# Kernel optimization log

Hardware: AMD Instinct MI355X
Metric: run time of the kernel (lower is better)

## Reference

```python
import jax, jax.numpy as jnp
import numpy as np

N = 10000          # total nodes
N_AGENTS = 5000    # drones (x[:, -1] < 0)
E = 160000         # random edges (self-loops added in reference)
C_IN, H, C_HID, C_OUT = 16, 8, 128, 8
NEG_SLOPE = 0.2    # GATv2Conv default leaky_relu slope


def setup_inputs() -> dict:
    key = jax.random.key(0)
    ks = jax.random.split(key, 12)
    x = jax.random.normal(ks[0], (N, C_IN), dtype=jnp.float32)
    # last feature column encodes node type: <0 -> drone, >=0 -> goal
    type_col = jnp.where(jnp.arange(N) < N_AGENTS, -1.0, 1.0).astype(jnp.float32)
    x = x.at[:, -1].set(type_col)
    edge_index = jax.random.randint(ks[1], (2, E), 0, N, dtype=jnp.int32)
    s = 0.1  # glorot-ish scale
    return {
        "x": x,
        "edge_index": edge_index,
        "Wl1": s * jax.random.normal(ks[2], (C_IN, H * C_HID), jnp.float32),
        "bl1": jnp.zeros((H * C_HID,), jnp.float32),
        "Wr1": s * jax.random.normal(ks[3], (C_IN, H * C_HID), jnp.float32),
        "br1": jnp.zeros((H * C_HID,), jnp.float32),
        "att1": s * jax.random.normal(ks[4], (H, C_HID), jnp.float32),
        "b1": jnp.zeros((C_HID,), jnp.float32),
        "Wl2": s * jax.random.normal(ks[5], (C_HID, H * C_HID), jnp.float32),
        "bl2": jnp.zeros((H * C_HID,), jnp.float32),
        "Wr2": s * jax.random.normal(ks[6], (C_HID, H * C_HID), jnp.float32),
        "br2": jnp.zeros((H * C_HID,), jnp.float32),
        "att2": s * jax.random.normal(ks[7], (H, C_HID), jnp.float32),
        "b2": jnp.zeros((C_HID,), jnp.float32),
        "Wlin": s * jax.random.normal(ks[8], (C_HID, C_OUT), jnp.float32),
        "blin": jnp.zeros((C_OUT,), jnp.float32),
    }


def gatv2_conv(x, src, dst, Wl, bl, Wr, br, att, bias):
    """PyG GATv2Conv, heads=H, concat=False (head-mean), add_self_loops handled by caller."""
    n = x.shape[0]
    xl = (x @ Wl + bl).reshape(n, H, -1)   # [N,H,C] source transform
    xr = (x @ Wr + br).reshape(n, H, -1)   # [N,H,C] target transform
    e = jax.nn.leaky_relu(xl[src] + xr[dst], NEG_SLOPE)          # [E,H,C]
    alpha = jnp.einsum("ehc,hc->eh", e, att)                      # [E,H]
    # per-destination softmax over incoming edges
    m = jax.ops.segment_max(alpha, dst, num_segments=n)
    a = jnp.exp(alpha - m[dst])
    denom = jax.ops.segment_sum(a, dst, num_segments=n)
    a = a / (denom[dst] + 1e-16)
    out = jax.ops.segment_sum(xl[src] * a[:, :, None], dst, num_segments=n)  # [N,H,C]
    return out.mean(axis=1) + bias  # concat=False -> mean over heads


def reference(x, edge_index, Wl1, bl1, Wr1, br1, att1, b1,
              Wl2, bl2, Wr2, br2, att2, b2, Wlin, blin):
    n = x.shape[0]
    loops = jnp.arange(n, dtype=edge_index.dtype)
    src = jnp.concatenate([edge_index[0], loops])
    dst = jnp.concatenate([edge_index[1], loops])
    drone_mask = x[:, -1] < 0
    y = x  # bounds is None -> no division
    h = jax.nn.relu(gatv2_conv(y, src, dst, Wl1, bl1, Wr1, br1, att1, b1))
    h = jax.nn.relu(gatv2_conv(h, src, dst, Wl2, bl2, Wr2, br2, att2, b2))
    out = h @ Wlin + blin  # [N, C_OUT]
    idx = jnp.nonzero(drone_mask, size=N_AGENTS)[0]
    return out[idx]  # [N_AGENTS, C_OUT]
```

## Files before the change

kernel.cpp:

```cpp
#include <hip/hip_runtime.h>
#include <hip/hip_fp16.h>
#include <math.h>

#define N_NODES 10000
#define N_EDGES 160000
#define NAG     5000
#define HC      1024
#define CH      128
#define NEG     0.2f
#define BCAP    64

#define NSCAT   625
#define NGEMM   1256

typedef _Float16 f16x8 __attribute__((ext_vector_type(8)));
typedef _Float16 f16x2 __attribute__((ext_vector_type(2)));
typedef float f32x4 __attribute__((ext_vector_type(4)));

__device__ __forceinline__ __half2 pk_max(__half2 a, __half2 b) {
    __half2 r;
    asm volatile("v_pk_max_f16 %0, %1, %2" : "=v"(r) : "v"(a), "v"(b));
    return r;
}

__device__ __forceinline__ void edge_accum(float4 raw, const __half2* xr2, const __half2* att2,
                                           float& lsum, float* acc, bool valid) {
    __half2* hp = (__half2*)&raw;
    const __half2 neg2 = __float2half2_rn(NEG);
    float p = 0.f;
    #pragma unroll
    for (int j = 0; j < 4; j++) {
        __half2 z = __hadd2(hp[j], xr2[j]);
        __half2 lz = pk_max(z, __hmul2(z, neg2));
#if __has_builtin(__builtin_amdgcn_fdot2)
        p = __builtin_amdgcn_fdot2(*(f16x2*)&lz, *(const f16x2*)&att2[j], p, false);
#else
        float2 lf = __half22float2(lz);
        float2 af = __half22float2(att2[j]);
        p = fmaf(lf.x, af.x, p);
        p = fmaf(lf.y, af.y, p);
#endif
    }
    p += __shfl_xor(p, 1, 64);
    p += __shfl_xor(p, 2, 64);
    p += __shfl_xor(p, 4, 64);
    p += __shfl_xor(p, 8, 64);
    float w = valid ? __expf(p) : 0.f;
    lsum += w;
    #pragma unroll
    for (int j = 0; j < 4; j++) {
        acc[2 * j]     = fmaf(__low2float(hp[j]),  w, acc[2 * j]);
        acc[2 * j + 1] = fmaf(__high2float(hp[j]), w, acc[2 * j + 1]);
    }
}

template <int K, int KA, typename AT>
__device__ void gemm_tile(char* smem, int vt,
                          const AT* __restrict__ A,
                          const _Float16* __restrict__ Whl, const float* __restrict__ bl,
                          const _Float16* __restrict__ Whr, const float* __restrict__ br,
                          _Float16* __restrict__ xl, _Float16* __restrict__ xr,
                          int limitL, int limitR) {
    _Float16* ash = (_Float16*)smem;
    float (*eps)[68] = (float(*)[68])smem;
    __shared__ float bsh[256];
    const int AS = K + 8;
    int by = vt & 7;
    int rowblk = (vt >> 3) * 64;
    bool right = by >= 4;
    if (rowblk >= (right ? limitR : limitL)) return;
    const _Float16* Wh = right ? Whr : Whl;
    const float* bs    = right ? br : bl;
    _Float16* outp     = right ? xr : xl;
    int colbase = (by & 3) * 256;
    int t = threadIdx.x;
    int w = t >> 6, l = t & 63;
    int m = l & 15, q = l >> 4;

    bsh[t] = bs[colbase + t];
    for (int idx = t; idx < 64 * (K / 8); idx += 256) {
        int r  = idx / (K / 8);
        int c8 = (idx % (K / 8)) * 8;
        int row = rowblk + r;
        f16x8 hv = (f16x8){0, 0, 0, 0, 0, 0, 0, 0};
        if (row < N_NODES && c8 < KA) {
            if constexpr (sizeof(AT) == 2) {
                hv = *(const f16x8*)((const _Float16*)A + (size_t)row * KA + c8);
            } else {
                float4 v0 = *(const float4*)((const float*)A + (size_t)row * KA + c8);
                float4 v1 = *(const float4*)((const float*)A + (size_t)row * KA + c8 + 4);
                hv[0] = (_Float16)v0.x; hv[1] = (_Float16)v0.y; hv[2] = (_Float16)v0.z; hv[3] = (_Float16)v0.w;
                hv[4] = (_Float16)v1.x; hv[5] = (_Float16)v1.y; hv[6] = (_Float16)v1.z; hv[7] = (_Float16)v1.w;
            }
        }
        *(f16x8*)&ash[r * AS + c8] = hv;
    }
    __syncthreads();

    f32x4 acc[16];
    #pragma unroll
    for (int i = 0; i < 16; i++) acc[i] = (f32x4){0.f, 0.f, 0.f, 0.f};

    #pragma unroll
    for (int kq = 0; kq < K / 32; kq++) {
        f16x8 af = *(const f16x8*)&ash[(w * 16 + m) * AS + kq * 32 + q * 8];
        const _Float16* base = Wh + (((size_t)(kq * 64 + (colbase >> 4))) << 9) + l * 8;
        #pragma unroll
        for (int tile = 0; tile < 16; tile++) {
            f16x8 bf = *(const f16x8*)(base + ((size_t)tile << 9));
            acc[tile] = __builtin_amdgcn_mfma_f32_16x16x32_f16(af, bf, acc[tile], 0, 0, 0);
        }
    }

    float bv[16];
    #pragma unroll
    for (int tile = 0; tile < 16; tile++) bv[tile] = bsh[tile * 16 + m];

    for (int cgk = 0; cgk < 4; cgk++) {
        __syncthreads();
        #pragma unroll
        for (int tt = 0; tt < 4; tt++) {
            int tile = cgk * 4 + tt;
            int cl = tt * 16 + m;
            #pragma unroll
            for (int reg = 0; reg < 4; reg++)
                eps[w * 16 + q * 4 + reg][cl] = acc[tile][reg] + bv[tile];
        }
        __syncthreads();
        int colg = colbase + cgk * 64;
        int cc = (t & 15) * 4;
        #pragma unroll
        for (int it = 0; it < 4; it++) {
            int r = it * 16 + (t >> 4);
            int row = rowblk + r;
            if (row < N_NODES) {
                float4 v = *(const float4*)&eps[r][cc];
                __half2 h01 = __floats2half2_rn(v.x, v.y);
                __half2 h23 = __floats2half2_rn(v.z, v.w);
                float2 st;
                st.x = *(float*)&h01;
                st.y = *(float*)&h23;
                *(float2*)(outp + (size_t)row * HC + colg + cc) = st;
            }
        }
    }
}

template <int LAYER>
__device__ void gat_phase(char* smem, int ndst,
                          const __half* __restrict__ xl, const _Float16* __restrict__ xr,
                          const float* __restrict__ att, const float* __restrict__ bias,
                          const int* __restrict__ cnt, const int* __restrict__ srcs,
                          _Float16* __restrict__ h_out,
                          const float* __restrict__ Wlin, const float* __restrict__ blin,
                          float* __restrict__ out) {
    float* part  = (float*)smem;
    float* lpart = (float*)(smem + 8192);
    float* hrow  = (float*)(smem + 8256);
    int t = threadIdx.x;
    int slot = t >> 7;
    int c0 = (t & 127) * 8;

    for (int dstn = blockIdx.x; dstn < ndst; dstn += gridDim.x) {
        __half2 xr2[4], att2[4];
        {
            f16x8 xv = *(const f16x8*)(xr + (size_t)dstn * HC + c0);
            __half2* xp = (__half2*)&xv;
            xr2[0] = xp[0]; xr2[1] = xp[1]; xr2[2] = xp[2]; xr2[3] = xp[3];
            float4 b0 = *(const float4*)(att + c0);
            float4 b1 = *(const float4*)(att + c0 + 4);
            att2[0] = __floats2half2_rn(b0.x, b0.y);
            att2[1] = __floats2half2_rn(b0.z, b0.w);
            att2[2] = __floats2half2_rn(b1.x, b1.y);
            att2[3] = __floats2half2_rn(b1.z, b1.w);
        }

        float acc[8];
        #pragma unroll
        for (int j = 0; j < 8; j++) acc[j] = 0.f;
        float lsum = 0.f;

        int e0 = dstn << 6;
        int e1 = e0 + cnt[dstn];
        int e = e0;
        for (; e + 16 <= e1; e += 16) {
            int s[8];
            #pragma unroll
            for (int i = 0; i < 8; i++) s[i] = srcs[e + slot + 2 * i];
            float4 raw[8];
            #pragma unroll
            for (int i = 0; i < 8; i++) raw[i] = *(const float4*)(xl + (size_t)s[i] * HC + c0);
            #pragma unroll
            for (int i = 0; i < 8; i++) edge_accum(raw[i], xr2, att2, lsum, acc, true);
        }
        for (; e + 4 <= e1; e += 4) {
            int s[2];
            #pragma unroll
            for (int i = 0; i < 2; i++) s[i] = srcs[e + slot + 2 * i];
            float4 raw[2];
            #pragma unroll
            for (int i = 0; i < 2; i++) raw[i] = *(const float4*)(xl + (size_t)s[i] * HC + c0);
            #pragma unroll
            for (int i = 0; i < 2; i++) edge_accum(raw[i], xr2, att2, lsum, acc, true);
        }
        for (; e < e1; e += 2) {
            int ee = e + slot;
            bool valid = ee < e1;
            int s = srcs[valid ? ee : e];
            float4 raw = *(const float4*)(xl + (size_t)s * HC + c0);
            edge_accum(raw, xr2, att2, lsum, acc, valid);
        }

        #pragma unroll
        for (int j = 0; j < 8; j++) part[slot * HC + c0 + j] = acc[j];
        if ((t & 15) == 0) lpart[slot * 8 + (c0 >> 7)] = lsum;
        __syncthreads();

        if (t < 128) {
            int head = t >> 4;
            float lv = lpart[head] + lpart[8 + head];
            float inv = 1.f / (lv + 1e-16f);
            #pragma unroll
            for (int j = 0; j < 8; j++) {
                int c = t * 8 + j;
                part[c] = (part[c] + part[HC + c]) * inv;
            }
        }
        __syncthreads();
        if (t < 128) {
            float ssum = 0.f;
            #pragma unroll
            for (int h = 0; h < 8; h++) ssum += part[h * 128 + t];
            float val = fmaxf(ssum * 0.125f + bias[t], 0.f);
            if (LAYER == 1) h_out[(size_t)dstn * CH + t] = (_Float16)val;
            else hrow[t] = val;
        }
        if (LAYER == 2) {
            __syncthreads();
            if (t < 64) {
                int j = t & 7, p8 = t >> 3;
                float v = 0.f;
                #pragma unroll
                for (int kk = 0; kk < 16; kk++) {
                    int k = p8 * 16 + kk;
                    v = fmaf(hrow[k], Wlin[k * 8 + j], v);
                }
                v += __shfl_xor(v, 8, 64);
                v += __shfl_xor(v, 16, 64);
                v += __shfl_xor(v, 32, 64);
                if (t < 8) out[(size_t)dstn * 8 + t] = v + blin[t];
            }
        }
        __syncthreads();
    }
}

__device__ __forceinline__ void emit_frag8(const float* __restrict__ W, _Float16* __restrict__ o,
                                           int tid, int KAreal) {
    int f = tid >> 6, l = tid & 63;
    int kq = f >> 6, tile = f & 63;
    int m = l & 15, q = l >> 4;
    int col = tile * 16 + m;
    float v[8];
    #pragma unroll
    for (int j = 0; j < 8; j++) {
        int k = kq * 32 + q * 8 + j;
        v[j] = (k < KAreal) ? W[k * 1024 + col] : 0.f;
    }
    f16x8 hv;
    #pragma unroll
    for (int j = 0; j < 8; j++) hv[j] = (_Float16)v[j];
    *(f16x8*)(o + ((size_t)tid << 3)) = hv;
}

__global__ __launch_bounds__(256) void prep_kernel(const float* __restrict__ Wl1, const float* __restrict__ Wr1,
                                                   const float* __restrict__ Wl2, const float* __restrict__ Wr2,
                                                   _Float16* __restrict__ w1l, _Float16* __restrict__ w1r,
                                                   _Float16* __restrict__ w2l, _Float16* __restrict__ w2r,
                                                   int* __restrict__ cnt, int* __restrict__ srcs) {
    int t = threadIdx.x;
    int b = blockIdx.x;
    if (b < 40) {
        int i = b * 256 + t;
        if (i < N_NODES) {
            cnt[i] = 1;
            srcs[i << 6] = i;
        }
        return;
    }
    if (b < 72) {
        int tid = (b - 40) * 256 + t;
        if (tid < 4096) emit_frag8(Wl1, w1l, tid, 16);
        else            emit_frag8(Wr1, w1r, tid - 4096, 16);
        return;
    }
    int tid = (b - 72) * 256 + t;
    if (tid < 16384) emit_frag8(Wl2, w2l, tid, 128);
    else             emit_frag8(Wr2, w2r, tid - 16384, 128);
}

__global__ __launch_bounds__(256) void d2_kernel(const int* __restrict__ esrc,
                                                 const int* __restrict__ edst,
                                                 int* __restrict__ cnt,
                                                 int* __restrict__ srcs,
                                                 const float* __restrict__ x,
                                                 const _Float16* __restrict__ w1l, const float* __restrict__ bl1,
                                                 const _Float16* __restrict__ w1r, const float* __restrict__ br1,
                                                 _Float16* __restrict__ xlh, _Float16* __restrict__ xrh) {
    __shared__ __align__(16) char smem[17408];
    int b = blockIdx.x;
    if (b < NGEMM) {
        gemm_tile<32, 16, float>(smem, b, x, w1l, bl1, w1r, br1,
                                 xlh, xrh, N_NODES, N_NODES);
    } else {
        int e = (b - NGEMM) * 256 + threadIdx.x;
        int d = edst[e];
        int p = atomicAdd(&cnt[d], 1);
        if (p < BCAP) srcs[(d << 6) + p] = esrc[e];
    }
}

__global__ __launch_bounds__(256) void gemm2_kernel(const _Float16* __restrict__ h1,
                                                    const _Float16* __restrict__ w2l, const float* __restrict__ bl2,
                                                    const _Float16* __restrict__ w2r, const float* __restrict__ br2,
                                                    _Float16* __restrict__ xlh, _Float16* __restrict__ xrh) {
    __shared__ __align__(16) char smem[17408];
    gemm_tile<128, 128, _Float16>(smem, blockIdx.x, h1, w2l, bl2, w2r, br2,
                                  xlh, xrh, N_NODES, NAG);
}

template <int LAYER>
__global__ __launch_bounds__(256) void gat_kernel(const __half* __restrict__ xl,
                                                  const _Float16* __restrict__ xr,
                                                  const float* __restrict__ att,
                                                  const float* __restrict__ bias,
                                                  const int* __restrict__ cnt,
                                                  const int* __restrict__ srcs,
                                                  _Float16* __restrict__ h_out,
                                                  const float* __restrict__ Wlin,
                                                  const float* __restrict__ blin,
                                                  float* __restrict__ out,
                                                  int ndst) {
    __shared__ __align__(16) char smem[8768];
    gat_phase<LAYER>(smem, ndst, xl, xr, att, bias, cnt, srcs, h_out, Wlin, blin, out);
}

extern "C" void kernel_launch(void* const* d_in, const int* in_sizes, int n_in,
                              void* d_out, int out_size, void* d_ws, size_t ws_size,
                              hipStream_t stream) {
    const float* x    = (const float*)d_in[0];
    const int*   ei   = (const int*)d_in[1];
    const float* Wl1  = (const float*)d_in[2];
    const float* bl1  = (const float*)d_in[3];
    const float* Wr1  = (const float*)d_in[4];
    const float* br1  = (const float*)d_in[5];
    const float* att1 = (const float*)d_in[6];
    const float* b1   = (const float*)d_in[7];
    const float* Wl2  = (const float*)d_in[8];
    const float* bl2  = (const float*)d_in[9];
    const float* Wr2  = (const float*)d_in[10];
    const float* br2  = (const float*)d_in[11];
    const float* att2 = (const float*)d_in[12];
    const float* b2   = (const float*)d_in[13];
    const float* Wlin = (const float*)d_in[14];
    const float* blin = (const float*)d_in[15];
    float* out = (float*)d_out;

    const int* esrc = ei;
    const int* edst = ei + N_EDGES;

    char* p = (char*)d_ws;
    __half* xlh    = (__half*)p;               p += (size_t)N_NODES * HC * sizeof(__half);
    _Float16* xrh  = (_Float16*)p;             p += (size_t)N_NODES * HC * sizeof(_Float16);
    _Float16* h1   = (_Float16*)p;             p += (size_t)N_NODES * CH * sizeof(_Float16);
    _Float16* w1l = (_Float16*)p;              p += 1024 * 32 * sizeof(_Float16);
    _Float16* w1r = (_Float16*)p;              p += 1024 * 32 * sizeof(_Float16);
    _Float16* w2l = (_Float16*)p;              p += 1024 * 128 * sizeof(_Float16);
    _Float16* w2r = (_Float16*)p;              p += 1024 * 128 * sizeof(_Float16);
    int* cnt  = (int*)p;                       p += (size_t)N_NODES * sizeof(int) + 64;
    int* srcs = (int*)p;

    prep_kernel<<<200, 256, 0, stream>>>(Wl1, Wr1, Wl2, Wr2, w1l, w1r, w2l, w2r, cnt, srcs);
    d2_kernel<<<NGEMM + NSCAT, 256, 0, stream>>>(esrc, edst, cnt, srcs, x,
                                                 w1l, bl1, w1r, br1,
                                                 (_Float16*)xlh, xrh);
    gat_kernel<1><<<N_NODES, 256, 0, stream>>>(xlh, xrh, att1, b1, cnt, srcs,
                                               h1, nullptr, nullptr, nullptr, N_NODES);
    gemm2_kernel<<<NGEMM, 256, 0, stream>>>(h1, w2l, bl2, w2r, br2, (_Float16*)xlh, xrh);
    gat_kernel<2><<<NAG, 256, 0, stream>>>(xlh, xrh, att2, b2, cnt, srcs,
                                           nullptr, Wlin, blin, out, NAG);
}
```

Baseline: 237.0 us.

## Split GAT aggregation per (dst, head) block and defer head-mean to consumers

The GAT aggregation kernel now launches one block per destination and head instead of one per destination. Each block's 16 edge slots cover 16 edges per iteration, so edge parallelism goes up and register pressure goes down. Per-head normalized outputs are written to a new [N,1024] fp16 buffer. The head-mean, bias and ReLU are folded into the layer-2 GEMM's A-tile load, and into a new small output kernel for layer 2. This adds extra global traffic for the per-head buffers, 8x more blocks, one extra launch, and a dropped unrolled gather loop, which lowers memory-level parallelism per thread.

```diff
diff --git a/kernel.cpp b/kernel.cpp
--- a/kernel.cpp
+++ b/kernel.cpp
@@ -54,9 +54,9 @@
     }
 }
 
-template <int K, int KA, typename AT>
+template <int K, int KA, bool TRANS, typename AT>
 __device__ void gemm_tile(char* smem, int vt,
-                          const AT* __restrict__ A,
+                          const AT* __restrict__ A, const float* __restrict__ tb,
                           const _Float16* __restrict__ Whl, const float* __restrict__ bl,
                           const _Float16* __restrict__ Whr, const float* __restrict__ br,
                           _Float16* __restrict__ xl, _Float16* __restrict__ xr,
@@ -84,7 +84,19 @@
         int row = rowblk + r;
         f16x8 hv = (f16x8){0, 0, 0, 0, 0, 0, 0, 0};
         if (row < N_NODES && c8 < KA) {
-            if constexpr (sizeof(AT) == 2) {
+            if constexpr (TRANS) {
+                f16x8 hvv[8];
+                #pragma unroll
+                for (int h = 0; h < 8; h++)
+                    hvv[h] = *(const f16x8*)((const _Float16*)A + (size_t)row * HC + h * CH + c8);
+                #pragma unroll
+                for (int j = 0; j < 8; j++) {
+                    float s = 0.f;
+                    #pragma unroll
+                    for (int h = 0; h < 8; h++) s += (float)hvv[h][j];
+                    hv[j] = (_Float16)fmaxf(fmaf(s, 0.125f, tb[c8 + j]), 0.f);
+                }
+            } else if constexpr (sizeof(AT) == 2) {
                 hv = *(const f16x8*)((const _Float16*)A + (size_t)row * KA + c8);
             } else {
                 float4 v0 = *(const float4*)((const float*)A + (size_t)row * KA + c8);
@@ -146,112 +158,89 @@
     }
 }
 
-template <int LAYER>
-__device__ void gat_phase(char* smem, int ndst,
-                          const __half* __restrict__ xl, const _Float16* __restrict__ xr,
-                          const float* __restrict__ att, const float* __restrict__ bias,
-                          const int* __restrict__ cnt, const int* __restrict__ srcs,
-                          _Float16* __restrict__ h_out,
-                          const float* __restrict__ Wlin, const float* __restrict__ blin,
-                          float* __restrict__ out) {
-    float* part  = (float*)smem;
-    float* lpart = (float*)(smem + 8192);
-    float* hrow  = (float*)(smem + 8256);
+__global__ __launch_bounds__(256) void gat_kernel(const __half* __restrict__ xl,
+                                                  const _Float16* __restrict__ xr,
+                                                  const float* __restrict__ att,
+                                                  const int* __restrict__ cnt,
+                                                  const int* __restrict__ srcs,
+                                                  _Float16* __restrict__ hpart) {
+    int b = blockIdx.x;
+    int dst = b >> 3, head = b & 7;
     int t = threadIdx.x;
-    int slot = t >> 7;
-    int c0 = (t & 127) * 8;
-
-    for (int dstn = blockIdx.x; dstn < ndst; dstn += gridDim.x) {
-        __half2 xr2[4], att2[4];
-        {
-            f16x8 xv = *(const f16x8*)(xr + (size_t)dstn * HC + c0);
-            __half2* xp = (__half2*)&xv;
-            xr2[0] = xp[0]; xr2[1] = xp[1]; xr2[2] = xp[2]; xr2[3] = xp[3];
-            float4 b0 = *(const float4*)(att + c0);
-            float4 b1 = *(const float4*)(att + c0 + 4);
-            att2[0] = __floats2half2_rn(b0.x, b0.y);
-            att2[1] = __floats2half2_rn(b0.z, b0.w);
-            att2[2] = __floats2half2_rn(b1.x, b1.y);
-            att2[3] = __floats2half2_rn(b1.z, b1.w);
-        }
-
-        float acc[8];
-        #pragma unroll
-        for (int j = 0; j < 8; j++) acc[j] = 0.f;
-        float lsum = 0.f;
-
-        int e0 = dstn << 6;
-        int e1 = e0 + cnt[dstn];
-        int e = e0;
-        for (; e + 16 <= e1; e += 16) {
-            int s[8];
-            #pragma unroll
-            for (int i = 0; i < 8; i++) s[i] = srcs[e + slot + 2 * i];
-            float4 raw[8];
-            #pragma unroll
-            for (int i = 0; i < 8; i++) raw[i] = *(const float4*)(xl + (size_t)s[i] * HC + c0);
-            #pragma unroll
-            for (int i = 0; i < 8; i++) edge_accum(raw[i], xr2, att2, lsum, acc, true);
-        }
-        for (; e + 4 <= e1; e += 4) {
-            int s[2];
-            #pragma unroll
-            for (int i = 0; i < 2; i++) s[i] = srcs[e + slot + 2 * i];
-            float4 raw[2];
-            #pragma unroll
-            for (int i = 0; i < 2; i++) raw[i] = *(const float4*)(xl + (size_t)s[i] * HC + c0);
-            #pragma unroll
-            for (int i = 0; i < 2; i++) edge_accum(raw[i], xr2, att2, lsum, acc, true);
-        }
-        for (; e < e1; e += 2) {
-            int ee = e + slot;
-            bool valid = ee < e1;
-            int s = srcs[valid ? ee : e];
-            float4 raw = *(const float4*)(xl + (size_t)s * HC + c0);
-            edge_accum(raw, xr2, att2, lsum, acc, valid);
-        }
-
-        #pragma unroll
-        for (int j = 0; j < 8; j++) part[slot * HC + c0 + j] = acc[j];
-        if ((t & 15) == 0) lpart[slot * 8 + (c0 >> 7)] = lsum;
-        __syncthreads();
-
-        if (t < 128) {
-            int head = t >> 4;
-            float lv = lpart[head] + lpart[8 + head];
-            float inv = 1.f / (lv + 1e-16f);
-            #pragma unroll
-            for (int j = 0; j < 8; j++) {
-                int c = t * 8 + j;
-                part[c] = (part[c] + part[HC + c]) * inv;
-            }
-        }
-        __syncthreads();
-        if (t < 128) {
-            float ssum = 0.f;
-            #pragma unroll
-            for (int h = 0; h < 8; h++) ssum += part[h * 128 + t];
-            float val = fmaxf(ssum * 0.125f + bias[t], 0.f);
-            if (LAYER == 1) h_out[(size_t)dstn * CH + t] = (_Float16)val;
-            else hrow[t] = val;
-        }
-        if (LAYER == 2) {
-            __syncthreads();
-            if (t < 64) {
-                int j = t & 7, p8 = t >> 3;
-                float v = 0.f;
-                #pragma unroll
-                for (int kk = 0; kk < 16; kk++) {
-                    int k = p8 * 16 + kk;
-                    v = fmaf(hrow[k], Wlin[k * 8 + j], v);
-                }
-                v += __shfl_xor(v, 8, 64);
-                v += __shfl_xor(v, 16, 64);
-                v += __shfl_xor(v, 32, 64);
-                if (t < 8) out[(size_t)dstn * 8 + t] = v + blin[t];
-            }
-        }
-        __syncthreads();
+    int slot = t >> 4, l16 = t & 15;
+    int ch0 = head * CH + l16 * 8;
+
+    __shared__ float part[16][128];
+    __shared__ float lslot[16];
+
+    __half2 xr2[4], att2[4];
+    {
+        f16x8 xv = *(const f16x8*)(xr + (size_t)dst * HC + ch0);
+        __half2* xp = (__half2*)&xv;
+        xr2[0] = xp[0]; xr2[1] = xp[1]; xr2[2] = xp[2]; xr2[3] = xp[3];
+        float4 b0 = *(const float4*)(att + ch0);
+        float4 b1 = *(const float4*)(att + ch0 + 4);
+        att2[0] = __floats2half2_rn(b0.x, b0.y);
+        att2[1] = __floats2half2_rn(b0.z, b0.w);
+        att2[2] = __floats2half2_rn(b1.x, b1.y);
+        att2[3] = __floats2half2_rn(b1.z, b1.w);
+    }
+
+    float acc[8];
+    #pragma unroll
+    for (int j = 0; j < 8; j++) acc[j] = 0.f;
+    float lsum = 0.f;
+
+    int e0 = dst << 6;
+    int e1 = e0 + cnt[dst];
+    for (int base = e0; base < e1; base += 16) {
+        int ee = base + slot;
+        bool valid = ee < e1;
+        int s = srcs[valid ? ee : e0];
+        float4 raw = *(const float4*)(xl + (size_t)s * HC + ch0);
+        edge_accum(raw, xr2, att2, lsum, acc, valid);
+    }
+
+    #pragma unroll
+    for (int j = 0; j < 8; j++) part[slot][l16 * 8 + j] = acc[j];
+    if (l16 == 0) lslot[slot] = lsum;
+    __syncthreads();
+
+    if (t < 128) {
+        float s = 0.f, lv = 0.f;
+        #pragma unroll
+        for (int k = 0; k < 16; k++) { s += part[k][t]; lv += lslot[k]; }
+        hpart[(size_t)dst * HC + head * CH + t] = (_Float16)(s / (lv + 1e-16f));
+    }
+}
+
+__global__ __launch_bounds__(256) void out_kernel(const _Float16* __restrict__ hpart2,
+                                                  const float* __restrict__ b2,
+                                                  const float* __restrict__ Wlin,
+                                                  const float* __restrict__ blin,
+                                                  float* __restrict__ out) {
+    int dst = blockIdx.x;
+    int t = threadIdx.x;
+    __shared__ float hrow[CH];
+    if (t < 128) {
+        float s = 0.f;
+        #pragma unroll
+        for (int h = 0; h < 8; h++) s += (float)hpart2[(size_t)dst * HC + h * CH + t];
+        hrow[t] = fmaxf(fmaf(s, 0.125f, b2[t]), 0.f);
+    }
+    __syncthreads();
+    if (t < 64) {
+        int j = t & 7, p8 = t >> 3;
+        float v = 0.f;
+        #pragma unroll
+        for (int kk = 0; kk < 16; kk++) {
+            int k = p8 * 16 + kk;
+            v = fmaf(hrow[k], Wlin[k * 8 + j], v);
+        }
+        v += __shfl_xor(v, 8, 64);
+        v += __shfl_xor(v, 16, 64);
+        v += __shfl_xor(v, 32, 64);
+        if (t < 8) out[(size_t)dst * 8 + t] = v + blin[t];
     }
 }
 
@@ -310,8 +299,8 @@
     __shared__ __align__(16) char smem[17408];
     int b = blockIdx.x;
     if (b < NGEMM) {
-        gemm_tile<32, 16, float>(smem, b, x, w1l, bl1, w1r, br1,
-                                 xlh, xrh, N_NODES, N_NODES);
+        gemm_tile<32, 16, false, float>(smem, b, x, nullptr, w1l, bl1, w1r, br1,
+                                        xlh, xrh, N_NODES, N_NODES);
     } else {
         int e = (b - NGEMM) * 256 + threadIdx.x;
         int d = edst[e];
@@ -320,29 +309,14 @@
     }
 }
 
-__global__ __launch_bounds__(256) void gemm2_kernel(const _Float16* __restrict__ h1,
+__global__ __launch_bounds__(256) void gemm2_kernel(const _Float16* __restrict__ hpart1,
+                                                    const float* __restrict__ b1,
                                                     const _Float16* __restrict__ w2l, const float* __restrict__ bl2,
                                                     const _Float16* __restrict__ w2r, const float* __restrict__ br2,
                                                     _Float16* __restrict__ xlh, _Float16* __restrict__ xrh) {
     __shared__ __align__(16) char smem[17408];
-    gemm_tile<128, 128, _Float16>(smem, blockIdx.x, h1, w2l, bl2, w2r, br2,
-                                  xlh, xrh, N_NODES, NAG);
-}
-
-template <int LAYER>
-__global__ __launch_bounds__(256) void gat_kernel(const __half* __restrict__ xl,
-                                                  const _Float16* __restrict__ xr,
-                                                  const float* __restrict__ att,
-                                                  const float* __restrict__ bias,
-                                                  const int* __restrict__ cnt,
-                                                  const int* __restrict__ srcs,
-                                                  _Float16* __restrict__ h_out,
-                                                  const float* __restrict__ Wlin,
-                                                  const float* __restrict__ blin,
-                                                  float* __restrict__ out,
-                                                  int ndst) {
-    __shared__ __align__(16) char smem[8768];
-    gat_phase<LAYER>(smem, ndst, xl, xr, att, bias, cnt, srcs, h_out, Wlin, blin, out);
+    gemm_tile<128, 128, true, _Float16>(smem, blockIdx.x, hpart1, b1, w2l, bl2, w2r, br2,
+                                        xlh, xrh, N_NODES, NAG);
 }
 
 extern "C" void kernel_launch(void* const* d_in, const int* in_sizes, int n_in,
@@ -372,7 +346,8 @@
     char* p = (char*)d_ws;
     __half* xlh    = (__half*)p;               p += (size_t)N_NODES * HC * sizeof(__half);
     _Float16* xrh  = (_Float16*)p;             p += (size_t)N_NODES * HC * sizeof(_Float16);
-    _Float16* h1   = (_Float16*)p;             p += (size_t)N_NODES * CH * sizeof(_Float16);
+    _Float16* hp1  = (_Float16*)p;             p += (size_t)N_NODES * HC * sizeof(_Float16);
+    _Float16* hp2  = (_Float16*)p;             p += (size_t)NAG * HC * sizeof(_Float16);
     _Float16* w1l = (_Float16*)p;              p += 1024 * 32 * sizeof(_Float16);
     _Float16* w1r = (_Float16*)p;              p += 1024 * 32 * sizeof(_Float16);
     _Float16* w2l = (_Float16*)p;              p += 1024 * 128 * sizeof(_Float16);
@@ -384,9 +359,9 @@
     d2_kernel<<<NGEMM + NSCAT, 256, 0, stream>>>(esrc, edst, cnt, srcs, x,
                                                  w1l, bl1, w1r, br1,
                                                  (_Float16*)xlh, xrh);
-    gat_kernel<1><<<N_NODES, 256, 0, stream>>>(xlh, xrh, att1, b1, cnt, srcs,
-                                               h1, nullptr, nullptr, nullptr, N_NODES);
-    gemm2_kernel<<<NGEMM, 256, 0, stream>>>(h1, w2l, bl2, w2r, br2, (_Float16*)xlh, xrh);
-    gat_kernel<2><<<NAG, 256, 0, stream>>>(xlh, xrh, att2, b2, cnt, srcs,
-                                           nullptr, Wlin, blin, out, NAG);
-}
+    gat_kernel<<<N_NODES * 8, 256, 0, stream>>>(xlh, xrh, att1, cnt, srcs, hp1);
+    gemm2_kernel<<<NGEMM, 256, 0, stream>>>(hp1, b1, w2l, bl2, w2r, br2,
+                                            (_Float16*)xlh, xrh);
+    gat_kernel<<<NAG * 8, 256, 0, stream>>>(xlh, xrh, att2, cnt, srcs, hp2);
+    out_kernel<<<NAG, 256, 0, stream>>>(hp2, b2, Wlin, blin, out);
+}
```

Measured after the change: 294.1 us. 24.1% more time.
